# Kernel optimization log

Measured on AMD Instinct MI355X. Metric: run time of the kernel, lower is better.

Reference implementation:

```python
import jax, jax.numpy as jnp
import numpy as np

COST_CLASS, COST_BBOX, COST_GIOU = 1.0, 5.0, 2.0
NUM_FRAMES, Q_PER_FRAME, NUM_TGT, NUM_CLASSES = 36, 100, 20, 92
B = 64


def box_cxcywh_to_xyxy(b):
    cx, cy, w, h = b[..., 0], b[..., 1], b[..., 2], b[..., 3]
    return jnp.stack([cx - 0.5 * w, cy - 0.5 * h, cx + 0.5 * w, cy + 0.5 * h], axis=-1)


def pairwise_giou(b1, b2):
    # b1: [..., Q, 4], b2: [..., T, 4], xyxy -> giou [..., Q, T]
    area1 = (b1[..., 2] - b1[..., 0]) * (b1[..., 3] - b1[..., 1])
    area2 = (b2[..., 2] - b2[..., 0]) * (b2[..., 3] - b2[..., 1])
    lt = jnp.maximum(b1[..., :, None, :2], b2[..., None, :, :2])
    rb = jnp.minimum(b1[..., :, None, 2:], b2[..., None, :, 2:])
    wh = jnp.clip(rb - lt, 0.0)
    inter = wh[..., 0] * wh[..., 1]
    union = area1[..., :, None] + area2[..., None, :] - inter
    iou = inter / union
    lt_e = jnp.minimum(b1[..., :, None, :2], b2[..., None, :, :2])
    rb_e = jnp.maximum(b1[..., :, None, 2:], b2[..., None, :, 2:])
    wh_e = jnp.clip(rb_e - lt_e, 0.0)
    area_e = wh_e[..., 0] * wh_e[..., 1]
    return iou - (area_e - union) / area_e


def compute_cost(pred_logits, pred_boxes, tgt_labels, tgt_boxes):
    b = pred_logits.shape[0]
    prob = jax.nn.softmax(pred_logits.reshape(b, NUM_FRAMES, Q_PER_FRAME, -1), axis=-1)  # [B,F,Q,C]
    pb = pred_boxes.reshape(b, NUM_FRAMES, Q_PER_FRAME, 4)
    lab = jnp.transpose(tgt_labels, (1, 0, 2))            # [B,F,T]
    tb = jnp.transpose(tgt_boxes, (1, 0, 2, 3))           # [B,F,T,4]
    onehot = jax.nn.one_hot(lab, prob.shape[-1], dtype=prob.dtype)  # [B,F,T,C]
    cost_class = -jnp.einsum('bfqc,bftc->bfqt', prob, onehot)
    cost_bbox = jnp.abs(pb[:, :, :, None, :] - tb[:, :, None, :, :]).sum(-1)  # L1 cdist
    giou = pairwise_giou(box_cxcywh_to_xyxy(pb), box_cxcywh_to_xyxy(tb))
    return COST_CLASS * cost_class + COST_BBOX * cost_bbox - COST_GIOU * giou


def auction_assign(cost):
    # cost [Q, T]; returns obj_of [T]: query index assigned to each target.
    # eps-optimal auction algorithm (replaces scipy linear_sum_assignment).
    Q, T = cost.shape
    benefit = -cost.T  # [T, Q]
    spread = jnp.max(benefit) - jnp.min(benefit) + 1e-6
    eps = spread / 1000.0
    neg_inf = jnp.asarray(-1e30, cost.dtype)

    def cond(s):
        _, _, obj_of, it = s
        return jnp.logical_and(jnp.any(obj_of < 0), it < 20000)

    def body(s):
        price, owner, obj_of, it = s
        unassigned = obj_of < 0                       # [T]
        vals = benefit - price[None, :]               # [T, Q]
        top2v, top2i = jax.lax.top_k(vals, 2)
        best_obj = top2i[:, 0]                        # [T]
        bid = price[best_obj] + (top2v[:, 0] - top2v[:, 1]) + eps
        bid = jnp.where(unassigned, bid, neg_inf)
        best_bid = jnp.full((Q,), neg_inf, cost.dtype).at[best_obj].max(bid)
        pids = jnp.arange(T, dtype=jnp.int32)
        win = unassigned & (bid >= best_bid[best_obj])
        winner = jnp.full((Q,), T, jnp.int32).at[best_obj].min(jnp.where(win, pids, T))
        has_bid = winner < T
        # evict previous owners of objects that received a bid
        evict = jnp.where(has_bid & (owner >= 0), owner, T)
        obj_of = obj_of.at[evict].set(-1, mode='drop')
        qids = jnp.arange(Q, dtype=jnp.int32)
        obj_of = obj_of.at[jnp.where(has_bid, winner, T)].set(jnp.where(has_bid, qids, -1), mode='drop')
        price = jnp.where(has_bid, best_bid, price)
        owner = jnp.where(has_bid, winner, owner)
        return price, owner, obj_of, it + 1

    init = (jnp.zeros((Q,), cost.dtype), jnp.full((Q,), -1, jnp.int32),
            jnp.full((T,), -1, jnp.int32), jnp.int32(0))
    _, _, obj_of, _ = jax.lax.while_loop(cond, body, init)
    return obj_of


def setup_inputs() -> dict:
    key = jax.random.key(0)
    k1, k2, k3, k4 = jax.random.split(key, 4)
    pred_logits = jax.random.normal(k1, (B, NUM_FRAMES * Q_PER_FRAME, NUM_CLASSES), jnp.float32)
    pred_boxes = jax.random.uniform(k2, (B, NUM_FRAMES * Q_PER_FRAME, 4), jnp.float32)
    tgt_labels = jax.random.randint(k3, (NUM_FRAMES, B, NUM_TGT), 0, NUM_CLASSES, jnp.int32)
    tgt_boxes = jax.random.uniform(k4, (NUM_FRAMES, B, NUM_TGT, 4), jnp.float32)
    return {'pred_logits': pred_logits, 'pred_boxes': pred_boxes,
            'tgt_labels': tgt_labels, 'tgt_boxes': tgt_boxes}


def reference(pred_logits, pred_boxes, tgt_labels, tgt_boxes):
    cost = compute_cost(pred_logits, pred_boxes, tgt_labels, tgt_boxes)  # [B,F,Q,T]
    b, f, q, t = cost.shape
    obj_of = jax.vmap(auction_assign)(cost.reshape(b * f, q, t))  # [BF, T]
    order = jnp.argsort(obj_of, axis=-1)  # scipy returns rows ascending
    pred_idx = jnp.take_along_axis(obj_of, order, axis=-1).reshape(b, f, t)
    tgt_idx = order.astype(jnp.int32).reshape(b, f, t)
    return cost, pred_idx, tgt_idx
```

## Files before the change

kernel.cpp:

```cpp
#include <hip/hip_runtime.h>

#define NF 36
#define QN 100
#define TN 20
#define CN 92
#define NB 64
#define BSTR 112

#define TOP2P(BV, PV, IDX) do { \
    float v_ = (BV) - (PV); bool c_ = v_ > v0; \
    float nv1_ = __builtin_amdgcn_fmed3f(v_, v0, v1); \
    i0 = c_ ? (IDX) : i0; p0 = c_ ? (PV) : p0; \
    v0 = fmaxf(v0, v_); v1 = nv1_; } while (0)

__global__ __launch_bounds__(64) void matcher_kernel(
    const float* __restrict__ logits,
    const float* __restrict__ pboxes,
    const int*   __restrict__ tlabels,
    const float* __restrict__ tboxes,
    float* __restrict__ out_cost,
    float* __restrict__ out_pred,
    float* __restrict__ out_tgt)
{
    const int bf = blockIdx.x;
    const int b  = bf / NF;
    const int f  = bf % NF;
    const int lane = threadIdx.x;

    __shared__ __align__(16) float ben[TN][BSTR];
    __shared__ __align__(16) float price[BSTR];
    __shared__ int   objl[TN];
    __shared__ int   slab[TN];
    __shared__ float tbr[TN][4];
    __shared__ float tbx[TN][4];
    __shared__ float tarea[TN];

    if (lane < TN) {
        const int base = (f * NB + b) * TN + lane;
        slab[lane] = tlabels[base];
        const float* tb = tboxes + (size_t)base * 4;
        float cx = tb[0], cy = tb[1], w = tb[2], h = tb[3];
        tbr[lane][0] = cx; tbr[lane][1] = cy; tbr[lane][2] = w; tbr[lane][3] = h;
        float x1 = cx - 0.5f * w, y1 = cy - 0.5f * h;
        float x2 = cx + 0.5f * w, y2 = cy + 0.5f * h;
        tbx[lane][0] = x1; tbx[lane][1] = y1; tbx[lane][2] = x2; tbx[lane][3] = y2;
        tarea[lane] = (x2 - x1) * (y2 - y1);
    }
    __syncthreads();

    float mn = INFINITY, mx = -INFINITY;
    for (int p = 0; p < 2; ++p) {
        const int q = lane + 64 * p;
        if (q < QN) {
            const size_t row = (size_t)b * (NF * QN) + (size_t)f * QN + q;
            const float* L = logits + row * CN;
            const float4* L4 = reinterpret_cast<const float4*>(L);

            float g[TN];
            #pragma unroll
            for (int t = 0; t < TN; ++t) g[t] = L[slab[t]];

            float m = -INFINITY, s = 0.f;
            #pragma unroll
            for (int i = 0; i < 23; ++i) {
                float4 v = L4[i];
                float cm = fmaxf(fmaxf(v.x, v.y), fmaxf(v.z, v.w));
                float m2 = fmaxf(m, cm);
                s = s * expf(m - m2)
                  + expf(v.x - m2) + expf(v.y - m2)
                  + expf(v.z - m2) + expf(v.w - m2);
                m = m2;
            }

            float4 pbv = reinterpret_cast<const float4*>(pboxes)[row];
            float cx = pbv.x, cy = pbv.y, w = pbv.z, h = pbv.w;
            float px1 = cx - 0.5f * w, py1 = cy - 0.5f * h;
            float px2 = cx + 0.5f * w, py2 = cy + 0.5f * h;
            float a1 = (px2 - px1) * (py2 - py1);

            for (int t = 0; t < TN; ++t) {
                float pc = expf(g[t] - m) / s;
                float cb = fabsf(cx - tbr[t][0]) + fabsf(cy - tbr[t][1]);
                cb = cb + fabsf(w - tbr[t][2]);
                cb = cb + fabsf(h - tbr[t][3]);
                float ltx = fmaxf(px1, tbx[t][0]), lty = fmaxf(py1, tbx[t][1]);
                float rbx = fminf(px2, tbx[t][2]), rby = fminf(py2, tbx[t][3]);
                float wx = fmaxf(rbx - ltx, 0.f), wy = fmaxf(rby - lty, 0.f);
                float inter = wx * wy;
                float uni = a1 + tarea[t] - inter;
                float iou = inter / uni;
                float ex1 = fminf(px1, tbx[t][0]), ey1 = fminf(py1, tbx[t][1]);
                float ex2 = fmaxf(px2, tbx[t][2]), ey2 = fmaxf(py2, tbx[t][3]);
                float ew = fmaxf(ex2 - ex1, 0.f), eh = fmaxf(ey2 - ey1, 0.f);
                float ae = ew * eh;
                float giou = iou - (ae - uni) / ae;
                float cost = (-pc) + 5.0f * cb - 2.0f * giou;
                ben[t][q] = -cost;
                mn = fminf(mn, cost);
                mx = fmaxf(mx, cost);
            }
        }
    }

    for (int i = lane; i < BSTR; i += 64) price[i] = 0.f;
    if (lane < TN) {
        float4 ninf; ninf.x = ninf.y = ninf.z = ninf.w = -INFINITY;
        float4* sp = reinterpret_cast<float4*>(&ben[lane][100]);
        sp[0] = ninf; sp[1] = ninf; sp[2] = ninf;
    }
    __syncthreads();

    #pragma unroll
    for (int off = 32; off > 0; off >>= 1) {
        mn = fminf(mn, __shfl_xor(mn, off, 64));
        mx = fmaxf(mx, __shfl_xor(mx, off, 64));
    }
    const float eps = (((-mn) - (-mx)) + 1e-6f) / 1000.0f;

    {
        float4* dst = reinterpret_cast<float4*>(out_cost + (size_t)bf * (QN * TN));
        for (int i = lane; i < (QN * TN) / 4; i += 64) {
            int k = i * 4;
            int q = k / TN, t0 = k - q * TN;
            float4 v;
            v.x = -ben[t0 + 0][q]; v.y = -ben[t0 + 1][q];
            v.z = -ben[t0 + 2][q]; v.w = -ben[t0 + 3][q];
            dst[i] = v;
        }
    }

    const int myt = lane / 3;
    const int jj  = lane - myt * 3;
    const int q0  = jj * 36;
    const bool is_leader = (lane < 60) && (jj == 0);
    float4 breg4[9];
    {
        const int tt = (lane < 60) ? myt : 0;
        const float4* bp = reinterpret_cast<const float4*>(&ben[tt][q0]);
        #pragma unroll
        for (int k = 0; k < 9; ++k) breg4[k] = bp[k];
    }
    int myobj = -1;

    for (int it = 0; it < 20000; ++it) {
        unsigned long long U = __ballot(is_leader && (myobj < 0));
        if (U == 0ull) break;
        const int u = __popcll(U);

        int bidq = 0; float bidf = 0.f;
        if (u > 2) {
            float v0 = -INFINITY, v1 = -INFINITY, p0 = 0.f; int i0 = q0;
            const float4* pp = reinterpret_cast<const float4*>(&price[q0]);
            #pragma unroll
            for (int k = 0; k < 9; ++k) {
                float4 bv = breg4[k];
                float4 pv = pp[k];
                TOP2P(bv.x, pv.x, q0 + 4*k + 0);
                TOP2P(bv.y, pv.y, q0 + 4*k + 1);
                TOP2P(bv.z, pv.z, q0 + 4*k + 2);
                TOP2P(bv.w, pv.w, q0 + 4*k + 3);
            }
            {
                float av0 = __shfl_down(v0, 1), av1 = __shfl_down(v1, 1), ap0 = __shfl_down(p0, 1);
                int   ai0 = __shfl_down(i0, 1);
                float bv0 = __shfl_down(v0, 2), bv1 = __shfl_down(v1, 2), bp0 = __shfl_down(p0, 2);
                int   bi0 = __shfl_down(i0, 2);
                if (av0 > v0) { v1 = fmaxf(v0, av1); v0 = av0; i0 = ai0; p0 = ap0; }
                else          { v1 = fmaxf(av0, v1); }
                if (bv0 > v0) { v1 = fmaxf(v0, bv1); v0 = bv0; i0 = bi0; p0 = bp0; }
                else          { v1 = fmaxf(bv0, v1); }
            }
            bidq = i0;
            bidf = p0 + (v0 - v1) + eps;
        } else {
            const int ta = (int)__builtin_ctzll(U) / 3;
            const int tb = (u == 2) ? (int)__builtin_ctzll(U & (U - 1ull)) / 3 : ta;
            const int grp = lane >> 5;
            const int tg  = grp ? tb : ta;
            const int l   = lane & 31;
            const int lc  = (l > 25) ? 25 : l;
            const int qb  = lc * 4;
            float4 bv = *reinterpret_cast<const float4*>(&ben[tg][qb]);
            float4 pv = *reinterpret_cast<const float4*>(&price[qb]);
            float v0 = -INFINITY, v1 = -INFINITY, p0 = 0.f; int i0 = qb;
            TOP2P(bv.x, pv.x, qb + 0);
            TOP2P(bv.y, pv.y, qb + 1);
            TOP2P(bv.z, pv.z, qb + 2);
            TOP2P(bv.w, pv.w, qb + 3);
            #pragma unroll
            for (int s = 16; s >= 1; s >>= 1) {
                float av0 = __shfl_xor(v0, s), av1 = __shfl_xor(v1, s), ap0 = __shfl_xor(p0, s);
                int   ai0 = __shfl_xor(i0, s);
                bool take = (av0 > v0) || (av0 == v0 && ai0 < i0);
                float nv1 = take ? fmaxf(v0, av1) : fmaxf(v1, av0);
                v0 = take ? av0 : v0;
                i0 = take ? ai0 : i0;
                p0 = take ? ap0 : p0;
                v1 = nv1;
            }
            float bidg = p0 + (v0 - v1) + eps;
            float b0 = __shfl(bidg, 0),  b1 = __shfl(bidg, 32);
            int   i0a = __shfl(i0, 0),   i0b = __shfl(i0, 32);
            if (lane == 3 * ta)            { bidq = i0a; bidf = b0; }
            if (u == 2 && lane == 3 * tb)  { bidq = i0b; bidf = b1; }
        }

        const bool act = is_leader && (myobj < 0);
        bool lose = false, ev = false;
        {
            unsigned long long uu = U;
            while (uu) {
                const int pos = (int)__builtin_ctzll(uu); uu &= uu - 1ull;
                const int t2  = pos / 3;
                const int   q2 = __builtin_amdgcn_readlane(bidq, pos);
                const float f2 = __int_as_float(__builtin_amdgcn_readlane(__float_as_int(bidf), pos));
                lose = lose || ((q2 == bidq) && ((f2 > bidf) || ((f2 == bidf) && (t2 < myt))));
                ev   = ev   || (q2 == myobj);
            }
        }
        if (act && !lose) {
            myobj = bidq;
            price[bidq] = bidf;
        } else if (ev) {
            myobj = -1;
        }
    }
    __syncthreads();
    if (is_leader) objl[myt] = myobj;
    __syncthreads();

    if (lane < TN) {
        int v = objl[lane];
        int r = 0;
        for (int u2 = 0; u2 < TN; ++u2) {
            int w = objl[u2];
            r += (w < v) || (w == v && u2 < lane);
        }
        out_pred[(size_t)bf * TN + r] = (float)v;
        out_tgt[(size_t)bf * TN + r]  = (float)lane;
    }
}

extern "C" void kernel_launch(void* const* d_in, const int* in_sizes, int n_in,
                              void* d_out, int out_size, void* d_ws, size_t ws_size,
                              hipStream_t stream) {
    const float* logits  = (const float*)d_in[0];
    const float* pboxes  = (const float*)d_in[1];
    const int*   tlabels = (const int*)d_in[2];
    const float* tboxes  = (const float*)d_in[3];

    float* out = (float*)d_out;
    float* out_cost = out;
    float* out_pred = out + (size_t)NB * NF * QN * TN;
    float* out_tgt  = out_pred + (size_t)NB * NF * TN;

    hipLaunchKernelGGL(matcher_kernel, dim3(NB * NF), dim3(64), 0, stream,
                       logits, pboxes, tlabels, tboxes, out_cost, out_pred, out_tgt);
}
```

Before: 180.3 us.

## Cache per-target top-8 benefit list to skip full price scans in auction

```diff
diff --git a/kernel.cpp b/kernel.cpp
--- a/kernel.cpp
+++ b/kernel.cpp
@@ -13,7 +13,28 @@
     i0 = c_ ? (IDX) : i0; p0 = c_ ? (PV) : p0; \
     v0 = fmaxf(v0, v_); v1 = nv1_; } while (0)
 
-__global__ __launch_bounds__(64) void matcher_kernel(
+#define LIST2(VAL, QI, PS) do { \
+    float v_ = (VAL); bool c_ = v_ > v0; bool e_ = (v_ == v0); \
+    v1 = c_ ? v0 : __builtin_amdgcn_fmed3f(v_, v0, v1); \
+    bool sw_ = c_ || (e_ && ((QI) < i0)); \
+    i0 = sw_ ? (QI) : i0; p0 = sw_ ? (PS) : p0; \
+    v0 = fmaxf(v0, v_); } while (0)
+
+#define INS8(VV, QQ) do { \
+    float v_ = (VV); \
+    bool c0_=v_>s8v[0], c1_=v_>s8v[1], c2_=v_>s8v[2], c3_=v_>s8v[3]; \
+    bool c4_=v_>s8v[4], c5_=v_>s8v[5], c6_=v_>s8v[6], c7_=v_>s8v[7]; \
+    s8v[7]=c6_?s8v[6]:(c7_?v_:s8v[7]); s8i[7]=c6_?s8i[6]:(c7_?(QQ):s8i[7]); \
+    s8v[6]=c5_?s8v[5]:(c6_?v_:s8v[6]); s8i[6]=c5_?s8i[5]:(c6_?(QQ):s8i[6]); \
+    s8v[5]=c4_?s8v[4]:(c5_?v_:s8v[5]); s8i[5]=c4_?s8i[4]:(c5_?(QQ):s8i[5]); \
+    s8v[4]=c3_?s8v[3]:(c4_?v_:s8v[4]); s8i[4]=c3_?s8i[3]:(c4_?(QQ):s8i[4]); \
+    s8v[3]=c2_?s8v[2]:(c3_?v_:s8v[3]); s8i[3]=c2_?s8i[2]:(c3_?(QQ):s8i[3]); \
+    s8v[2]=c1_?s8v[1]:(c2_?v_:s8v[2]); s8i[2]=c1_?s8i[1]:(c2_?(QQ):s8i[2]); \
+    s8v[1]=c0_?s8v[0]:(c1_?v_:s8v[1]); s8i[1]=c0_?s8i[0]:(c1_?(QQ):s8i[1]); \
+    s8v[0]=c0_?v_:s8v[0];              s8i[0]=c0_?(QQ):s8i[0]; \
+} while (0)
+
+__global__ __launch_bounds__(64, 2) void matcher_kernel(
     const float* __restrict__ logits,
     const float* __restrict__ pboxes,
     const int*   __restrict__ tlabels,
@@ -142,23 +163,73 @@
     }
     int myobj = -1;
 
+    float s8v[8]; int s8i[8];
+    #pragma unroll
+    for (int j = 0; j < 8; ++j) { s8v[j] = -INFINITY; s8i[j] = 0; }
+    #pragma unroll
+    for (int k = 0; k < 9; ++k) {
+        float4 bv = breg4[k];
+        INS8(bv.x, q0 + 4*k + 0);
+        INS8(bv.y, q0 + 4*k + 1);
+        INS8(bv.z, q0 + 4*k + 2);
+        INS8(bv.w, q0 + 4*k + 3);
+    }
+    {
+        float av[8], bw[8]; int ai[8], bi[8];
+        #pragma unroll
+        for (int j = 0; j < 8; ++j) {
+            av[j] = __shfl_down(s8v[j], 1); ai[j] = __shfl_down(s8i[j], 1);
+            bw[j] = __shfl_down(s8v[j], 2); bi[j] = __shfl_down(s8i[j], 2);
+        }
+        #pragma unroll
+        for (int j = 0; j < 8; ++j) INS8(av[j], ai[j]);
+        #pragma unroll
+        for (int j = 0; j < 8; ++j) INS8(bw[j], bi[j]);
+    }
+    const float lB = s8v[7];
+    float pv[8];
+    #pragma unroll
+    for (int j = 0; j < 8; ++j) pv[j] = 0.f;
+    bool lvalid = true;
+
     for (int it = 0; it < 20000; ++it) {
         unsigned long long U = __ballot(is_leader && (myobj < 0));
         if (U == 0ull) break;
-        const int u = __popcll(U);
 
         int bidq = 0; float bidf = 0.f;
-        if (u > 2) {
+        const bool act = is_leader && (myobj < 0);
+
+        if (act && lvalid) {
+            float v0 = -INFINITY, v1 = -INFINITY, p0 = 0.f; int i0 = 0;
+            #pragma unroll
+            for (int j = 0; j < 8; ++j) {
+                float pj = pv[j];
+                LIST2(s8v[j] - pj, s8i[j], pj);
+            }
+            if ((v0 > lB) && (v1 >= lB)) {
+                bidq = i0;
+                bidf = p0 + (v0 - v1) + eps;
+            } else {
+                lvalid = false;
+            }
+        }
+
+        unsigned long long R = __ballot(is_leader && (myobj < 0) && !lvalid);
+
+        if (R != 0ull) {
+            const bool doscan = (lane < 60) && (((R >> (3 * myt)) & 1ull) != 0ull);
             float v0 = -INFINITY, v1 = -INFINITY, p0 = 0.f; int i0 = q0;
-            const float4* pp = reinterpret_cast<const float4*>(&price[q0]);
-            #pragma unroll
-            for (int k = 0; k < 9; ++k) {
-                float4 bv = breg4[k];
-                float4 pv = pp[k];
-                TOP2P(bv.x, pv.x, q0 + 4*k + 0);
-                TOP2P(bv.y, pv.y, q0 + 4*k + 1);
-                TOP2P(bv.z, pv.z, q0 + 4*k + 2);
-                TOP2P(bv.w, pv.w, q0 + 4*k + 3);
+            if (doscan) {
+                const float4* pp = reinterpret_cast<const float4*>(&price[q0]);
+                #pragma unroll
+                for (int k = 0; k < 9; ++k) {
+                    float4 bv = breg4[k];
+                    float4 pvv = pp[k];
+                    TOP2P(bv.x, pvv.x, q0 + 4*k + 0);
+                    TOP2P(bv.y, pvv.y, q0 + 4*k + 1);
+                    TOP2P(bv.z, pvv.z, q0 + 4*k + 2);
+                    TOP2P(bv.w, pvv.w, q0 + 4*k + 3);
+                }
             }
             {
                 float av0 = __shfl_down(v0, 1), av1 = __shfl_down(v1, 1), ap0 = __shfl_down(p0, 1);
@@ -170,42 +241,12 @@
                 if (bv0 > v0) { v1 = fmaxf(v0, bv1); v0 = bv0; i0 = bi0; p0 = bp0; }
                 else          { v1 = fmaxf(bv0, v1); }
             }
-            bidq = i0;
-            bidf = p0 + (v0 - v1) + eps;
-        } else {
-            const int ta = (int)__builtin_ctzll(U) / 3;
-            const int tb = (u == 2) ? (int)__builtin_ctzll(U & (U - 1ull)) / 3 : ta;
-            const int grp = lane >> 5;
-            const int tg  = grp ? tb : ta;
-            const int l   = lane & 31;
-            const int lc  = (l > 25) ? 25 : l;
-            const int qb  = lc * 4;
-            float4 bv = *reinterpret_cast<const float4*>(&ben[tg][qb]);
-            float4 pv = *reinterpret_cast<const float4*>(&price[qb]);
-            float v0 = -INFINITY, v1 = -INFINITY, p0 = 0.f; int i0 = qb;
-            TOP2P(bv.x, pv.x, qb + 0);
-            TOP2P(bv.y, pv.y, qb + 1);
-            TOP2P(bv.z, pv.z, qb + 2);
-            TOP2P(bv.w, pv.w, qb + 3);
-            #pragma unroll
-            for (int s = 16; s >= 1; s >>= 1) {
-                float av0 = __shfl_xor(v0, s), av1 = __shfl_xor(v1, s), ap0 = __shfl_xor(p0, s);
-                int   ai0 = __shfl_xor(i0, s);
-                bool take = (av0 > v0) || (av0 == v0 && ai0 < i0);
-                float nv1 = take ? fmaxf(v0, av1) : fmaxf(v1, av0);
-                v0 = take ? av0 : v0;
-                i0 = take ? ai0 : i0;
-                p0 = take ? ap0 : p0;
-                v1 = nv1;
-            }
-            float bidg = p0 + (v0 - v1) + eps;
-            float b0 = __shfl(bidg, 0),  b1 = __shfl(bidg, 32);
-            int   i0a = __shfl(i0, 0),   i0b = __shfl(i0, 32);
-            if (lane == 3 * ta)            { bidq = i0a; bidf = b0; }
-            if (u == 2 && lane == 3 * tb)  { bidq = i0b; bidf = b1; }
-        }
-
-        const bool act = is_leader && (myobj < 0);
+            if (is_leader && (((R >> lane) & 1ull) != 0ull)) {
+                bidq = i0;
+                bidf = p0 + (v0 - v1) + eps;
+            }
+        }
+
         bool lose = false, ev = false;
         {
             unsigned long long uu = U;
@@ -216,6 +257,9 @@
                 const float f2 = __int_as_float(__builtin_amdgcn_readlane(__float_as_int(bidf), pos));
                 lose = lose || ((q2 == bidq) && ((f2 > bidf) || ((f2 == bidf) && (t2 < myt))));
                 ev   = ev   || (q2 == myobj);
+                #pragma unroll
+                for (int j = 0; j < 8; ++j)
+                    pv[j] = (q2 == s8i[j]) ? fmaxf(pv[j], f2) : pv[j];
             }
         }
         if (act && !lose) {
```

Result: slower. 188.2 us (+4.4%).
